# Performance work log

Hardware: AMD Instinct MI355X
Metric: run time of the kernel (lower is better)

Reference implementation:

```python
import jax, jax.numpy as jnp
import numpy as np

B, L, D = 8, 4096, 1024
MAX_CHUNKS = 128
BOUNDARY_P = 0.03  # ~123 boundaries per sequence, just under max_chunks


def setup_inputs() -> dict:
    key = jax.random.key(0)
    kx, kb = jax.random.split(key)
    x = jax.random.normal(kx, (B, L, D), dtype=jnp.float32)
    # float 'boundary probabilities'; forward thresholds at 0.5 -> produce 0/1 floats
    boundaries = (jax.random.uniform(kb, (B, L)) < BOUNDARY_P).astype(jnp.float32)
    return {"x": x, "boundaries": boundaries}


def reference(x, boundaries):
    """Vectorized equivalent of ChunkLayer.forward.

    Chunk i of a sequence spans [b_i, b_{i+1}) for consecutive boundary
    positions (last chunk runs to seq end). Tokens before the first
    boundary get segment id -1 and are dropped, matching the torch loop.
    Output is mean-pooled chunks, zero-padded/truncated to MAX_CHUNKS.
    """
    Bb, Ll, Dd = x.shape
    bmask = (boundaries > 0.5).astype(jnp.int32)          # [B, L]
    seg = jnp.cumsum(bmask, axis=1) - 1                   # [B, L], -1 before first boundary
    # route dropped (seg<0) and overflow (seg>=MAX_CHUNKS) tokens to a trash segment
    seg = jnp.where((seg < 0) | (seg >= MAX_CHUNKS), MAX_CHUNKS, seg)

    def per_batch(xi, si):
        sums = jax.ops.segment_sum(xi, si, num_segments=MAX_CHUNKS + 1)[:MAX_CHUNKS]       # [C, D]
        cnts = jax.ops.segment_sum(jnp.ones((Ll,), xi.dtype), si,
                                   num_segments=MAX_CHUNKS + 1)[:MAX_CHUNKS]               # [C]
        return sums, cnts

    sums, cnts = jax.vmap(per_batch)(x, seg)              # [B, C, D], [B, C]
    means = jnp.where(cnts[..., None] > 0,
                      sums / jnp.maximum(cnts, 1.0)[..., None],
                      0.0)                                # zero-pad empty chunks
    return means, cnts.astype(jnp.int32)
```

## Files before the change

kernel.cpp:

```cpp
#include <hip/hip_runtime.h>

#define B_DIM 8
#define L_DIM 4096
#define D_DIM 1024
#define MAXC 128
#define RG 4
#define CT 256

__device__ __forceinline__ void f4add(float4& a, const float4& v) {
    a.x += v.x; a.y += v.y; a.z += v.z; a.w += v.w;
}

__global__ __launch_bounds__(1024)
void fused_chunk_kernel(const float* __restrict__ x,
                        const float* __restrict__ bnd,
                        float* __restrict__ out_means,
                        float* __restrict__ out_cnts)
{
    const int bc = blockIdx.x;
    const int b  = bc >> 7;
    const int c  = bc & (MAXC - 1);
    const int t  = threadIdx.x;
    const int tc = t & (CT - 1);
    const int rg = t >> 8;

    __shared__ int s[256];
    __shared__ int sb[2];
    __shared__ float4 red[RG][CT];

    if (t == 0) { sb[0] = 0; sb[1] = L_DIM; }

    unsigned m = 0u;
    int cnt16 = 0;
    if (t < 256) {
        const float* p = bnd + (size_t)b * L_DIM + t * 16;
        const float4* p4 = reinterpret_cast<const float4*>(p);
#pragma unroll
        for (int q = 0; q < 4; ++q) {
            float4 v = p4[q];
            if (v.x > 0.5f) m |= 1u << (q * 4 + 0);
            if (v.y > 0.5f) m |= 1u << (q * 4 + 1);
            if (v.z > 0.5f) m |= 1u << (q * 4 + 2);
            if (v.w > 0.5f) m |= 1u << (q * 4 + 3);
        }
        cnt16 = __popc(m);
        s[t] = cnt16;
    }
    __syncthreads();
    for (int off = 1; off < 256; off <<= 1) {
        int v = (t >= off && t < 256) ? s[t - off] : 0;
        __syncthreads();
        if (t < 256) s[t] += v;
        __syncthreads();
    }
    const int n = s[255];
    if (t < 256 && m != 0u) {
        int idx = s[t] - cnt16;
        const int base = t * 16;
#pragma unroll
        for (int j = 0; j < 16; ++j) {
            if (m & (1u << j)) {
                if (idx == c)     sb[0] = base + j;
                if (idx == c + 1) sb[1] = base + j;
                ++idx;
            }
        }
    }
    __syncthreads();

    int cnt = 0;
    float4 a0 = make_float4(0.f, 0.f, 0.f, 0.f);
    float4 a1 = a0, a2 = a0, a3 = a0, a4 = a0, a5 = a0, a6 = a0, a7 = a0;

    if (c < n) {
        const int start = sb[0];
        const int end   = sb[1];
        cnt = end - start;

        const int nr = (cnt - rg + RG - 1) / RG;
        const float* xp = x + ((size_t)b * L_DIM + start + rg) * D_DIM + tc * 4;
        const size_t stride = (size_t)RG * D_DIM;

        int k = 0;
        const int rem = nr & 7;
        if (rem & 4) {
            float4 v0 = *reinterpret_cast<const float4*>(xp + (size_t)(k + 0) * stride);
            float4 v1 = *reinterpret_cast<const float4*>(xp + (size_t)(k + 1) * stride);
            float4 v2 = *reinterpret_cast<const float4*>(xp + (size_t)(k + 2) * stride);
            float4 v3 = *reinterpret_cast<const float4*>(xp + (size_t)(k + 3) * stride);
            f4add(a0, v0); f4add(a1, v1); f4add(a2, v2); f4add(a3, v3);
            k += 4;
        }
        if (rem & 2) {
            float4 v0 = *reinterpret_cast<const float4*>(xp + (size_t)(k + 0) * stride);
            float4 v1 = *reinterpret_cast<const float4*>(xp + (size_t)(k + 1) * stride);
            f4add(a4, v0); f4add(a5, v1);
            k += 2;
        }
        if (rem & 1) {
            float4 v0 = *reinterpret_cast<const float4*>(xp + (size_t)k * stride);
            f4add(a6, v0);
            k += 1;
        }
        for (; k + 8 <= nr; k += 8) {
            const float* base = xp + (size_t)k * stride;
            float4 v0 = *reinterpret_cast<const float4*>(base + 0 * stride);
            float4 v1 = *reinterpret_cast<const float4*>(base + 1 * stride);
            float4 v2 = *reinterpret_cast<const float4*>(base + 2 * stride);
            float4 v3 = *reinterpret_cast<const float4*>(base + 3 * stride);
            float4 v4 = *reinterpret_cast<const float4*>(base + 4 * stride);
            float4 v5 = *reinterpret_cast<const float4*>(base + 5 * stride);
            float4 v6 = *reinterpret_cast<const float4*>(base + 6 * stride);
            float4 v7 = *reinterpret_cast<const float4*>(base + 7 * stride);
            f4add(a0, v0); f4add(a1, v1); f4add(a2, v2); f4add(a3, v3);
            f4add(a4, v4); f4add(a5, v5); f4add(a6, v6); f4add(a7, v7);
        }
        f4add(a0, a1); f4add(a2, a3); f4add(a4, a5); f4add(a6, a7);
        f4add(a0, a2); f4add(a4, a6);
        f4add(a0, a4);
    }

    red[rg][tc] = a0;
    __syncthreads();

    if (t < CT) {
        float4 s0 = red[0][t];
        f4add(s0, red[1][t]);
        f4add(s0, red[2][t]);
        f4add(s0, red[3][t]);
        const float inv = (cnt > 0) ? (1.0f / (float)cnt) : 0.0f;
        s0.x *= inv; s0.y *= inv; s0.z *= inv; s0.w *= inv;
        float4* op = reinterpret_cast<float4*>(out_means + (size_t)bc * D_DIM) + t;
        *op = s0;
        if (t == 0) out_cnts[bc] = (float)cnt;
    }
}

extern "C" void kernel_launch(void* const* d_in, const int* in_sizes, int n_in,
                              void* d_out, int out_size, void* d_ws, size_t ws_size,
                              hipStream_t stream)
{
    const float* x   = (const float*)d_in[0];
    const float* bnd = (const float*)d_in[1];

    float* out = (float*)d_out;
    float* out_means = out;
    float* out_cnts  = out + (size_t)B_DIM * MAXC * D_DIM;

    fused_chunk_kernel<<<B_DIM * MAXC, 1024, 0, stream>>>(x, bnd,
                                                          out_means, out_cnts);
}
```

Baseline: 31.82 us.

## Use wave-shuffle scan over all threads for boundary prefix sum, trim accumulators

Replaces the 256-thread shared-memory Hillis-Steele scan, which needed many block barriers, with a per-wave shuffle scan across all 1024 threads plus a 16-entry wave-total combine. Each thread now handles 4 boundary flags instead of 16. The accumulation loop uses 4 accumulators instead of 8, and the remainder rows move after the main loop. Launch bounds also request 8 waves per SIMD, which pressures the register budget.

```diff
diff --git a/kernel.cpp b/kernel.cpp
--- a/kernel.cpp
+++ b/kernel.cpp
@@ -11,54 +11,57 @@
     a.x += v.x; a.y += v.y; a.z += v.z; a.w += v.w;
 }
 
-__global__ __launch_bounds__(1024)
+__global__ __launch_bounds__(1024, 8)
 void fused_chunk_kernel(const float* __restrict__ x,
                         const float* __restrict__ bnd,
                         float* __restrict__ out_means,
                         float* __restrict__ out_cnts)
 {
-    const int bc = blockIdx.x;
-    const int b  = bc >> 7;
-    const int c  = bc & (MAXC - 1);
-    const int t  = threadIdx.x;
-    const int tc = t & (CT - 1);
-    const int rg = t >> 8;
+    const int bc   = blockIdx.x;
+    const int b    = bc >> 7;
+    const int c    = bc & (MAXC - 1);
+    const int t    = threadIdx.x;
+    const int tc   = t & (CT - 1);
+    const int rg   = t >> 8;
+    const int lane = t & 63;
+    const int w    = t >> 6;
 
-    __shared__ int s[256];
+    __shared__ int wtot[16];
     __shared__ int sb[2];
     __shared__ float4 red[RG][CT];
 
     if (t == 0) { sb[0] = 0; sb[1] = L_DIM; }
 
+    const float4 bv = reinterpret_cast<const float4*>(bnd + (size_t)b * L_DIM)[t];
     unsigned m = 0u;
-    int cnt16 = 0;
-    if (t < 256) {
-        const float* p = bnd + (size_t)b * L_DIM + t * 16;
-        const float4* p4 = reinterpret_cast<const float4*>(p);
+    if (bv.x > 0.5f) m |= 1u;
+    if (bv.y > 0.5f) m |= 2u;
+    if (bv.z > 0.5f) m |= 4u;
+    if (bv.w > 0.5f) m |= 8u;
+    const int cnt4 = __popc(m);
+
+    int incl = cnt4;
 #pragma unroll
-        for (int q = 0; q < 4; ++q) {
-            float4 v = p4[q];
-            if (v.x > 0.5f) m |= 1u << (q * 4 + 0);
-            if (v.y > 0.5f) m |= 1u << (q * 4 + 1);
-            if (v.z > 0.5f) m |= 1u << (q * 4 + 2);
-            if (v.w > 0.5f) m |= 1u << (q * 4 + 3);
-        }
-        cnt16 = __popc(m);
-        s[t] = cnt16;
+    for (int off = 1; off < 64; off <<= 1) {
+        int u = __shfl_up(incl, off, 64);
+        if (lane >= off) incl += u;
     }
+    if (lane == 63) wtot[w] = incl;
     __syncthreads();
-    for (int off = 1; off < 256; off <<= 1) {
-        int v = (t >= off && t < 256) ? s[t - off] : 0;
-        __syncthreads();
-        if (t < 256) s[t] += v;
-        __syncthreads();
+
+    int waveoff = 0, n = 0;
+#pragma unroll
+    for (int i = 0; i < 16; ++i) {
+        const int ww = wtot[i];
+        n += ww;
+        if (i < w) waveoff += ww;
     }
-    const int n = s[255];
-    if (t < 256 && m != 0u) {
-        int idx = s[t] - cnt16;
-        const int base = t * 16;
+
+    if (m != 0u) {
+        int idx = waveoff + incl - cnt4;
+        const int base = t * 4;
 #pragma unroll
-        for (int j = 0; j < 16; ++j) {
+        for (int j = 0; j < 4; ++j) {
             if (m & (1u << j)) {
                 if (idx == c)     sb[0] = base + j;
                 if (idx == c + 1) sb[1] = base + j;
@@ -70,7 +73,7 @@
 
     int cnt = 0;
     float4 a0 = make_float4(0.f, 0.f, 0.f, 0.f);
-    float4 a1 = a0, a2 = a0, a3 = a0, a4 = a0, a5 = a0, a6 = a0, a7 = a0;
+    float4 a1 = a0, a2 = a0, a3 = a0;
 
     if (c < n) {
         const int start = sb[0];
@@ -82,26 +85,6 @@
         const size_t stride = (size_t)RG * D_DIM;
 
         int k = 0;
-        const int rem = nr & 7;
-        if (rem & 4) {
-            float4 v0 = *reinterpret_cast<const float4*>(xp + (size_t)(k + 0) * stride);
-            float4 v1 = *reinterpret_cast<const float4*>(xp + (size_t)(k + 1) * stride);
-            float4 v2 = *reinterpret_cast<const float4*>(xp + (size_t)(k + 2) * stride);
-            float4 v3 = *reinterpret_cast<const float4*>(xp + (size_t)(k + 3) * stride);
-            f4add(a0, v0); f4add(a1, v1); f4add(a2, v2); f4add(a3, v3);
-            k += 4;
-        }
-        if (rem & 2) {
-            float4 v0 = *reinterpret_cast<const float4*>(xp + (size_t)(k + 0) * stride);
-            float4 v1 = *reinterpret_cast<const float4*>(xp + (size_t)(k + 1) * stride);
-            f4add(a4, v0); f4add(a5, v1);
-            k += 2;
-        }
-        if (rem & 1) {
-            float4 v0 = *reinterpret_cast<const float4*>(xp + (size_t)k * stride);
-            f4add(a6, v0);
-            k += 1;
-        }
         for (; k + 8 <= nr; k += 8) {
             const float* base = xp + (size_t)k * stride;
             float4 v0 = *reinterpret_cast<const float4*>(base + 0 * stride);
@@ -113,11 +96,29 @@
             float4 v6 = *reinterpret_cast<const float4*>(base + 6 * stride);
             float4 v7 = *reinterpret_cast<const float4*>(base + 7 * stride);
             f4add(a0, v0); f4add(a1, v1); f4add(a2, v2); f4add(a3, v3);
-            f4add(a4, v4); f4add(a5, v5); f4add(a6, v6); f4add(a7, v7);
+            f4add(a0, v4); f4add(a1, v5); f4add(a2, v6); f4add(a3, v7);
         }
-        f4add(a0, a1); f4add(a2, a3); f4add(a4, a5); f4add(a6, a7);
-        f4add(a0, a2); f4add(a4, a6);
-        f4add(a0, a4);
+        if (k + 4 <= nr) {
+            const float* base = xp + (size_t)k * stride;
+            float4 v0 = *reinterpret_cast<const float4*>(base + 0 * stride);
+            float4 v1 = *reinterpret_cast<const float4*>(base + 1 * stride);
+            float4 v2 = *reinterpret_cast<const float4*>(base + 2 * stride);
+            float4 v3 = *reinterpret_cast<const float4*>(base + 3 * stride);
+            f4add(a0, v0); f4add(a1, v1); f4add(a2, v2); f4add(a3, v3);
+            k += 4;
+        }
+        if (k + 2 <= nr) {
+            const float* base = xp + (size_t)k * stride;
+            float4 v0 = *reinterpret_cast<const float4*>(base + 0 * stride);
+            float4 v1 = *reinterpret_cast<const float4*>(base + 1 * stride);
+            f4add(a0, v0); f4add(a1, v1);
+            k += 2;
+        }
+        if (k < nr) {
+            f4add(a2, *reinterpret_cast<const float4*>(xp + (size_t)k * stride));
+        }
+        f4add(a0, a1); f4add(a2, a3);
+        f4add(a0, a2);
     }
 
     red[rg][tc] = a0;
```

Measured after the change: 31.65 us. Within noise of the previous version (-0.5%).
